# Optimization experiments

Measured on AMD Instinct MI355X. Metric: run time of the kernel, lower is better.

Reference implementation:

```python
import jax, jax.numpy as jnp
import numpy as np

# dims matching init_kwargs
B, N = 1, 2048
VOCAB, DIM, DEPTH = 32000, 1024, 4
HEADS, DIM_HEAD, WINDOW = 16, 64, 512
INNER = HEADS * DIM_HEAD          # 1024
FF_INNER = int(DIM * 4 * 2 / 3)   # 2730 (GEGLU inner)
DPB_DIM = DIM // 2
LN_EPS = 1e-5


def layernorm(x, g, b):
    m = jnp.mean(x, axis=-1, keepdims=True)
    v = jnp.mean(jnp.square(x - m), axis=-1, keepdims=True)
    return (x - m) * jax.lax.rsqrt(v + LN_EPS) * g + b


def look_around(x, backward=1, forward=0, pad_value=-1):
    # x: [b, nw, w, ...]; concat shifted windows along the window_size axis
    nw = x.shape[1]
    pads = [(0, 0), (backward, forward)] + [(0, 0)] * (x.ndim - 2)
    px = jnp.pad(x, pads, constant_values=pad_value)
    return jnp.concatenate([px[:, i:i + nw] for i in range(backward + forward + 1)], axis=2)


def dynamic_pos_bias(w1, b1, w2, b2, w3, b3, i, j):
    # MLP over scalar relative distances, then gather into [H, i, j]
    rel = jnp.arange(j, dtype=jnp.float32)[:, None]            # [j, 1]
    h = jax.nn.silu(rel @ w1 + b1)
    h = jax.nn.silu(h @ w2 + b2)
    bias = h @ w3 + b3                                          # [j, H]
    idx = jnp.abs(jnp.arange(j - i, j)[:, None] - jnp.arange(j)[None, :])  # [i, j]
    return jnp.transpose(bias[idx], (2, 0, 1))                  # [H, i, j]


def local_attention(q, k, v, attn_bias):
    # causal sliding-window attention, look_backward=1, look_forward=0, exact_windowsize=True
    # q,k,v: [B,H,N,dh]; N assumed multiple of WINDOW (autopad is a no-op then)
    b, h, n, d = q.shape
    w = WINDOW
    nw = n // w
    scale = d ** -0.5
    bq = q.reshape(b * h, nw, w, d) * scale
    bk = look_around(k.reshape(b * h, nw, w, d), pad_value=-1.0)   # [bh,nw,2w,d]
    bv = look_around(v.reshape(b * h, nw, w, d), pad_value=-1.0)
    t = jnp.arange(n).reshape(1, nw, w)
    bq_t = t[..., :, None]                                      # [1,nw,w,1]
    bq_k = look_around(t, pad_value=-1)[..., None, :]           # [1,nw,1,2w]
    # causal | exact-window | padding masks
    mask = (bq_t < bq_k) | (bq_t > bq_k + w) | (bq_k == -1)
    sim = jnp.einsum('bwid,bwjd->bwij', bq, bk)                 # [bh,nw,w,2w]
    sim = (sim.reshape(b, h, nw, w, 2 * w) + attn_bias[None, :, None]).reshape(b * h, nw, w, 2 * w)
    sim = jnp.where(mask, -jnp.finfo(sim.dtype).max, sim)
    attn = jax.nn.softmax(sim, axis=-1)
    out = jnp.einsum('bwij,bwjd->bwid', attn, bv)
    return out.reshape(b, h, n, d)


def forward(tokens, tok_emb, pos_emb, dpb_w1, dpb_b1, dpb_w2, dpb_b2, dpb_w3, dpb_b3,
            ln1_g, ln1_b, Wqkv, Wo, ln2_g, ln2_b, Wff1, Wff2, lnf_g, lnf_b, Wlogits):
    bsz, n = tokens.shape
    x = tok_emb[tokens] + pos_emb[:n]                           # [B,N,D]
    bias = dynamic_pos_bias(dpb_w1, dpb_b1, dpb_w2, dpb_b2, dpb_w3, dpb_b3, WINDOW, 2 * WINDOW)

    def split_heads(t):
        return t.reshape(bsz, n, HEADS, DIM_HEAD).transpose(0, 2, 1, 3)

    for l in range(DEPTH):
        # LocalMHA (prenorm) + residual
        h = layernorm(x, ln1_g[l], ln1_b[l])
        q, k, v = jnp.split(h @ Wqkv[l], 3, axis=-1)
        o = local_attention(split_heads(q), split_heads(k), split_heads(v), bias)
        o = o.transpose(0, 2, 1, 3).reshape(bsz, n, INNER)
        x = x + o @ Wo[l]
        # GEGLU FFN (prenorm inside FeedForward) + residual
        h = layernorm(x, ln2_g[l], ln2_b[l])
        a, gate = jnp.split(h @ Wff1[l], 2, axis=-1)
        x = x + (a * jax.nn.gelu(gate, approximate=False)) @ Wff2[l]

    return layernorm(x, lnf_g, lnf_b) @ Wlogits                 # [B,N,V]


def setup_inputs() -> dict:
    key = jax.random.key(0)
    ks = iter(jax.random.split(key, 16))
    s = 0.02
    rn = lambda *shape: jax.random.normal(next(ks), shape, dtype=jnp.float32) * s
    return {
        'tokens': jax.random.randint(next(ks), (B, N), 0, VOCAB, dtype=jnp.int32),
        'tok_emb': rn(VOCAB, DIM),
        'pos_emb': rn(N, DIM),
        'dpb_w1': rn(1, DPB_DIM), 'dpb_b1': jnp.zeros((DPB_DIM,), jnp.float32),
        'dpb_w2': rn(DPB_DIM, DPB_DIM), 'dpb_b2': jnp.zeros((DPB_DIM,), jnp.float32),
        'dpb_w3': rn(DPB_DIM, HEADS), 'dpb_b3': jnp.zeros((HEADS,), jnp.float32),
        'ln1_g': jnp.ones((DEPTH, DIM), jnp.float32), 'ln1_b': jnp.zeros((DEPTH, DIM), jnp.float32),
        'Wqkv': rn(DEPTH, DIM, 3 * INNER),
        'Wo': rn(DEPTH, INNER, DIM),
        'ln2_g': jnp.ones((DEPTH, DIM), jnp.float32), 'ln2_b': jnp.zeros((DEPTH, DIM), jnp.float32),
        'Wff1': rn(DEPTH, DIM, 2 * FF_INNER),
        'Wff2': rn(DEPTH, FF_INNER, DIM),
        'lnf_g': jnp.ones((DIM,), jnp.float32), 'lnf_b': jnp.zeros((DIM,), jnp.float32),
        'Wlogits': rn(DIM, VOCAB),
    }


def reference(tokens, tok_emb, pos_emb, dpb_w1, dpb_b1, dpb_w2, dpb_b2, dpb_w3, dpb_b3,
              ln1_g, ln1_b, Wqkv, Wo, ln2_g, ln2_b, Wff1, Wff2, lnf_g, lnf_b, Wlogits):
    return forward(tokens, tok_emb, pos_emb, dpb_w1, dpb_b1, dpb_w2, dpb_b2, dpb_w3, dpb_b3,
                   ln1_g, ln1_b, Wqkv, Wo, ln2_g, ln2_b, Wff1, Wff2, lnf_g, lnf_b, Wlogits)
```

## Files before the change

### kernel.cpp

```cpp
#include <hip/hip_runtime.h>
#include <cstdint>

#define DEV __device__ __forceinline__

typedef __attribute__((ext_vector_type(8))) short bf16x8;
typedef __attribute__((ext_vector_type(4))) short bf16x4;
typedef __attribute__((ext_vector_type(4))) float f32x4;
typedef __attribute__((ext_vector_type(8))) unsigned short u16x8;

DEV float bf2f(unsigned short u) { return __uint_as_float(((unsigned)u) << 16); }
DEV unsigned short f2bf(float f) {
  unsigned u = __float_as_uint(f);
  u += 0x7FFFu + ((u >> 16) & 1u);
  return (unsigned short)(u >> 16);
}

DEV void gload_lds16(const void* g, void* lds) {
  __builtin_amdgcn_global_load_lds(
      (const __attribute__((address_space(1))) unsigned int*)g,
      (__attribute__((address_space(3))) unsigned int*)lds, 16, 0, 0);
}

__global__ __launch_bounds__(256) void k_prep(
    const int* __restrict__ tokens, const float* __restrict__ tok_emb,
    const float* __restrict__ pos_emb, float* __restrict__ x,
    const float* __restrict__ w1, const float* __restrict__ b1,
    const float* __restrict__ w2, const float* __restrict__ b2,
    const float* __restrict__ w3, const float* __restrict__ b3,
    float* __restrict__ tableT,
    const float* __restrict__ Wqkv, unsigned short* __restrict__ WqkvT,
    const float* __restrict__ Wo, unsigned short* __restrict__ WoT,
    const float* __restrict__ Wff1, unsigned short* __restrict__ Wff1T,
    const float* __restrict__ Wff2, unsigned short* __restrict__ Wff2T,
    const float* __restrict__ Wlog, unsigned short* __restrict__ WlogT) {
  __shared__ unsigned short sm16[8192];
  int b = blockIdx.x, t = threadIdx.x;
  if (b < 2048) {
    int tok = tokens[b];
    int c = t * 4;
    float4 a = *(const float4*)(tok_emb + (long)tok * 1024 + c);
    float4 p = *(const float4*)(pos_emb + (long)b * 1024 + c);
    float4 r;
    r.x = a.x + p.x; r.y = a.y + p.y; r.z = a.z + p.z; r.w = a.w + p.w;
    *(float4*)(x + (long)b * 1024 + c) = r;
    return;
  }
  b -= 2048;
  if (b < 1024) {
    float* h1 = (float*)sm16;
    float* h2 = h1 + 512;
    float rf = (float)b;
    for (int c = t; c < 512; c += 256) {
      float v = rf * w1[c] + b1[c];
      h1[c] = v / (1.0f + __expf(-v));
    }
    __syncthreads();
    for (int c = t; c < 512; c += 256) {
      float acc = b2[c];
      for (int k2 = 0; k2 < 512; ++k2) acc = fmaf(h1[k2], w2[(long)k2 * 512 + c], acc);
      h2[c] = acc / (1.0f + __expf(-acc));
    }
    __syncthreads();
    if (t < 16) {
      float acc = b3[t];
      for (int k2 = 0; k2 < 512; ++k2) acc = fmaf(h2[k2], w3[k2 * 16 + t], acc);
      tableT[t * 1024 + b] = acc;
    }
    return;
  }
  b -= 1024;
  const float* src; unsigned short* dst;
  int N, Kreal, nt, kt, mode;
  if (b < 1536) {
    int z = b / 384, r = b % 384;
    nt = r / 16; kt = r % 16; mode = 0; N = 3072; Kreal = 1024;
    src = Wqkv + (long)z * 1024 * 3072;
    dst = WqkvT + ((long)z * 384 + r) * 8192;
  } else if ((b -= 1536) < 512) {
    int z = b / 128, r = b % 128;
    nt = r / 16; kt = r % 16; mode = 0; N = 1024; Kreal = 1024;
    src = Wo + (long)z * 1024 * 1024;
    dst = WoT + ((long)z * 128 + r) * 8192;
  } else if ((b -= 512) < 2752) {
    int z = b / 688, r = b % 688;
    nt = r / 16; kt = r % 16; mode = 1; N = 5460; Kreal = 1024;
    src = Wff1 + (long)z * 1024 * 5460;
    dst = Wff1T + ((long)z * 688 + r) * 8192;
  } else if ((b -= 2752) < 1376) {
    int z = b / 344, r = b % 344;
    nt = r / 43; kt = r % 43; mode = 0; N = 1024; Kreal = 2730;
    src = Wff2 + (long)z * 2730 * 1024;
    dst = Wff2T + ((long)z * 344 + r) * 8192;
  } else {
    b -= 1376;
    nt = b / 16; kt = b % 16; mode = 0; N = 32000; Kreal = 1024;
    src = Wlog;
    dst = WlogT + (long)b * 8192;
  }
  const int k0 = kt * 64;
  const int q = t & 31;
  const int kc = t >> 5;
  u16x8 pa, pb, pc, pd;
  if (mode == 0) {
    const int nb = nt * 128 + q * 4;
    float4 v[8];
#pragma unroll
    for (int e = 0; e < 8; ++e) {
      int k = k0 + kc * 8 + e;
      float4 tmp = {0.f, 0.f, 0.f, 0.f};
      if (k < Kreal) tmp = *(const float4*)(src + (long)k * N + nb);
      v[e] = tmp;
    }
    __builtin_amdgcn_sched_barrier(0);
#pragma unroll
    for (int e = 0; e < 8; ++e) {
      pa[e] = f2bf(v[e].x); pb[e] = f2bf(v[e].y);
      pc[e] = f2bf(v[e].z); pd[e] = f2bf(v[e].w);
    }
  } else {
    const int f0 = nt * 64 + q * 2;
    float2 av[8], gv[8];
#pragma unroll
    for (int e = 0; e < 8; ++e) {
      int k = k0 + kc * 8 + e;
      const float* sr = src + (long)k * 5460;
      float2 af = {0.f, 0.f}, gf = {0.f, 0.f};
      if (f0 + 1 < 2730) {
        af = *(const float2*)(sr + f0);
        gf = *(const float2*)(sr + 2730 + f0);
      } else if (f0 < 2730) {
        af.x = sr[f0];
        gf.x = sr[2730 + f0];
      }
      av[e] = af; gv[e] = gf;
    }
    __builtin_amdgcn_sched_barrier(0);
#pragma unroll
    for (int e = 0; e < 8; ++e) {
      pa[e] = f2bf(av[e].x); pb[e] = f2bf(gv[e].x);
      pc[e] = f2bf(av[e].y); pd[e] = f2bf(gv[e].y);
    }
  }
  {
    const int r0 = q * 4;
    *(u16x8*)&sm16[(r0 + 0) * 64 + ((kc ^ ((r0 + 0) & 7)) * 8)] = pa;
    *(u16x8*)&sm16[(r0 + 1) * 64 + ((kc ^ ((r0 + 1) & 7)) * 8)] = pb;
    *(u16x8*)&sm16[(r0 + 2) * 64 + ((kc ^ ((r0 + 2) & 7)) * 8)] = pc;
    *(u16x8*)&sm16[(r0 + 3) * 64 + ((kc ^ ((r0 + 3) & 7)) * 8)] = pd;
  }
  __syncthreads();
#pragma unroll
  for (int i2 = 0; i2 < 4; ++i2)
    *(u16x8*)(dst + i2 * 2048 + t * 8) = *(const u16x8*)&sm16[i2 * 2048 + t * 8];
}

__global__ __launch_bounds__(256) void k_ln4(const float* __restrict__ x,
    const float* __restrict__ g, const float* __restrict__ b,
    unsigned short* __restrict__ out) {
  const int row = blockIdx.x * 4 + (threadIdx.x >> 6);
  const int l = threadIdx.x & 63;
  const float* xr = x + (long)row * 1024 + l * 16;
  float4 v[4];
#pragma unroll
  for (int e = 0; e < 4; ++e) v[e] = ((const float4*)xr)[e];
  float s = 0.0f;
#pragma unroll
  for (int e = 0; e < 4; ++e) s += v[e].x + v[e].y + v[e].z + v[e].w;
#pragma unroll
  for (int off = 32; off; off >>= 1) s += __shfl_xor(s, off);
  float mean = s * (1.0f / 1024.0f);
  float sq = 0.0f;
#pragma unroll
  for (int e = 0; e < 4; ++e) {
    float a0 = v[e].x - mean, a1 = v[e].y - mean, a2 = v[e].z - mean, a3 = v[e].w - mean;
    sq += a0 * a0 + a1 * a1 + a2 * a2 + a3 * a3;
  }
#pragma unroll
  for (int off = 32; off; off >>= 1) sq += __shfl_xor(sq, off);
  float inv = rsqrtf(sq * (1.0f / 1024.0f) + 1e-5f);
  const float* gr = g + l * 16;
  const float* br = b + l * 16;
  unsigned short* orow = out + (long)row * 1024 + l * 16;
#pragma unroll
  for (int e = 0; e < 4; ++e) {
    float4 gv = ((const float4*)gr)[e];
    float4 bv = ((const float4*)br)[e];
    ushort4 o;
    o.x = f2bf((v[e].x - mean) * inv * gv.x + bv.x);
    o.y = f2bf((v[e].y - mean) * inv * gv.y + bv.y);
    o.z = f2bf((v[e].z - mean) * inv * gv.z + bv.z);
    o.w = f2bf((v[e].w - mean) * inv * gv.w + bv.w);
    ((ushort4*)orow)[e] = o;
  }
}

__global__ __launch_bounds__(256, 2) void k_attn_mfma(
    const unsigned short* __restrict__ qkv, const float* __restrict__ tableT,
    unsigned short* __restrict__ o) {
  __shared__ unsigned short Ks[64 * 64];
  __shared__ unsigned short Vt[64 * 72];
  __shared__ unsigned short Ps[4][16 * 72];
  __shared__ float biasl[1024];
  const int qt = blockIdx.x, h = blockIdx.y, wi = blockIdx.z;
  const int iw0 = qt * 64;
  const int t = threadIdx.x;
  const int w = t >> 6, l = t & 63;
  const int lq = l & 15, lk = l >> 4;

  *(float4*)&biasl[t * 4] = *(const float4*)(tableT + h * 1024 + t * 4);

  const unsigned short* qp = qkv + (long)(wi * 512 + iw0 + w * 16 + lq) * 3072 + h * 64;
  bf16x8 qf0 = *(const bf16x8*)(qp + lk * 8);
  bf16x8 qf1 = *(const bf16x8*)(qp + 32 + lk * 8);

  f32x4 oacc[4] = {};
  float mrun[4] = {-3.0e38f, -3.0e38f, -3.0e38f, -3.0e38f};
  float srun[4] = {};

  const int kt0 = (wi == 0) ? 8 : qt;
  const int kt1 = qt + 8;
  for (int kt = kt0; kt <= kt1; ++kt) {
    const int ktbase = kt * 64;
    const long kgbase = (long)((wi - 1) * 512 + ktbase);
    __syncthreads();
    {
      const unsigned short* Kg = qkv + kgbase * 3072 + 1024 + h * 64;
#pragma unroll
      for (int s2 = 0; s2 < 2; ++s2) {
        int g = s2 * 4 + w;
        int row = g * 8 + (l >> 3);
        int gch = (l & 7) ^ (row & 7);
        gload_lds16(Kg + (long)row * 3072 + gch * 8, &Ks[g * 512]);
      }
    }
    {
      int kp = t & 31, dg = t >> 5;
      const unsigned short* Vg =
          qkv + (kgbase + 2 * kp) * 3072 + 2048 + h * 64 + dg * 8;
      bf16x8 a0 = *(const bf16x8*)Vg;
      bf16x8 a1 = *(const bf16x8*)(Vg + 3072);
#pragma unroll
      for (int e = 0; e < 8; ++e) {
        unsigned pack = ((unsigned)(unsigned short)a0[e]) |
                        (((unsigned)(unsigned short)a1[e]) << 16);
        *(unsigned*)&Vt[(dg * 8 + e) * 72 + 2 * kp] = pack;
      }
    }
    asm volatile("s_waitcnt vmcnt(0)" ::: "memory");
    __syncthreads();

    f32x4 sacc[4] = {};
#pragma unroll
    for (int ct = 0; ct < 4; ++ct) {
      int krow = ct * 16 + lq;
      bf16x8 kf0 = *(const bf16x8*)&Ks[krow * 64 + (((0 + lk) ^ (krow & 7)) * 8)];
      bf16x8 kf1 = *(const bf16x8*)&Ks[krow * 64 + (((4 + lk) ^ (krow & 7)) * 8)];
      sacc[ct] = __builtin_amdgcn_mfma_f32_16x16x32_bf16(qf0, kf0, sacc[ct], 0, 0, 0);
      sacc[ct] = __builtin_amdgcn_mfma_f32_16x16x32_bf16(qf1, kf1, sacc[ct], 0, 0, 0);
    }

#pragma unroll
    for (int r = 0; r < 4; ++r) {
      const int iw = iw0 + w * 16 + lk * 4 + r;
      float sc[4];
#pragma unroll
      for (int ct = 0; ct < 4; ++ct) {
        int jj = ktbase + ct * 16 + lq;
        int di = 512 + iw - jj;
        int dic = min(max(di, 0), 1023);
        bool allowed = (jj >= iw) && (jj <= iw + 512);
        float v = sacc[ct][r] * 0.125f + biasl[dic];
        sc[ct] = allowed ? v : -3.0e38f;
      }
      float mx = fmaxf(fmaxf(sc[0], sc[1]), fmaxf(sc[2], sc[3]));
      mx = fmaxf(mx, __shfl_xor(mx, 1));
      mx = fmaxf(mx, __shfl_xor(mx, 2));
      mx = fmaxf(mx, __shfl_xor(mx, 4));
      mx = fmaxf(mx, __shfl_xor(mx, 8));
      float mnew = fmaxf(mrun[r], mx);
      float f = __expf(mrun[r] - mnew);
      mrun[r] = mnew;
      float rs = 0.0f;
#pragma unroll
      for (int ct = 0; ct < 4; ++ct) {
        float pv = __expf(sc[ct] - mnew);
        rs += pv;
        Ps[w][(lk * 4 + r) * 72 + ct * 16 + lq] = f2bf(pv);
      }
      rs += __shfl_xor(rs, 1);
      rs += __shfl_xor(rs, 2);
      rs += __shfl_xor(rs, 4);
      rs += __shfl_xor(rs, 8);
      srun[r] = srun[r] * f + rs;
#pragma unroll
      for (int dt = 0; dt < 4; ++dt) oacc[dt][r] *= f;
    }
    asm volatile("s_waitcnt lgkmcnt(0)" ::: "memory");

#pragma unroll
    for (int ks = 0; ks < 2; ++ks) {
      bf16x4 pa0 = *(const bf16x4*)&Ps[w][lq * 72 + ks * 32 + lk * 8];
      bf16x4 pa1 = *(const bf16x4*)&Ps[w][lq * 72 + ks * 32 + lk * 8 + 4];
      bf16x8 pa = __builtin_shufflevector(pa0, pa1, 0, 1, 2, 3, 4, 5, 6, 7);
#pragma unroll
      for (int dt = 0; dt < 4; ++dt) {
        int drow = dt * 16 + lq;
        bf16x4 vb0 = *(const bf16x4*)&Vt[drow * 72 + ks * 32 + lk * 8];
        bf16x4 vb1 = *(const bf16x4*)&Vt[drow * 72 + ks * 32 + lk * 8 + 4];
        bf16x8 vb = __builtin_shufflevector(vb0, vb1, 0, 1, 2, 3, 4, 5, 6, 7);
        oacc[dt] = __builtin_amdgcn_mfma_f32_16x16x32_bf16(pa, vb, oacc[dt], 0, 0, 0);
      }
    }
  }

  unsigned short* ob =
      o + (long)(wi * 512 + iw0 + w * 16 + lk * 4) * 1024 + h * 64 + lq;
#pragma unroll
  for (int r = 0; r < 4; ++r) {
    float inv = 1.0f / srun[r];
#pragma unroll
    for (int dt = 0; dt < 4; ++dt)
      ob[(long)r * 1024 + dt * 16] = f2bf(oacc[dt][r] * inv);
  }
}

template <int EPI, int BM>
__global__ __launch_bounds__(256, 2) void k_gemm(const unsigned short* __restrict__ A,
    const unsigned short* __restrict__ BTt, void* __restrict__ Cout,
    int N, int K, int nbm) {
  constexpr int MI = BM / 32;
  __shared__ unsigned short As[BM * 64];
  __shared__ unsigned short Bs[128 * 64];
  const int nwg = gridDim.x;
  const int orig = blockIdx.x;
  const int q8 = nwg >> 3, r8 = nwg & 7;
  const int xcd = orig & 7, i8 = orig >> 3;
  const int wgid = (xcd < r8 ? xcd * (q8 + 1) : r8 * (q8 + 1) + (xcd - r8) * q8) + i8;
  const int bm = wgid % nbm;
  const int bn = wgid / nbm;
  const int t = threadIdx.x;
  const int w = t >> 6, l = t & 63;
  const int wm = w >> 1, wn = w & 1;
  const int lrow = l >> 3, lch = l & 7;
  const int lq = l & 15, lk = l >> 4;
  f32x4 acc[MI][4] = {};
  const long arow0 = (long)bm * BM;
  const unsigned short* btile = BTt + (long)bn * (K >> 6) * 8192;
  for (int kt = 0; kt < K; kt += 64) {
    __syncthreads();
    const unsigned short* bsrc = btile + (long)(kt >> 6) * 8192 + l * 8;
#pragma unroll
    for (int s2 = 0; s2 < 4; ++s2) {
      int grp = s2 * 4 + w;
      gload_lds16(bsrc + grp * 512, &Bs[grp * 512]);
      if (s2 < MI) {
        int r = grp * 8 + lrow;
        int gch = lch ^ lrow;
        gload_lds16(A + (arow0 + r) * K + kt + gch * 8, &As[grp * 512]);
      }
    }
    asm volatile("s_waitcnt vmcnt(0)" ::: "memory");
    __syncthreads();
#pragma unroll
    for (int kk = 0; kk < 2; ++kk) {
      bf16x8 af[MI], bfr[4];
#pragma unroll
      for (int i = 0; i < MI; ++i) {
        int ra = wm * (BM / 2) + i * 16 + lq;
        af[i] = *(const bf16x8*)&As[ra * 64 + (((kk * 4 + lk) ^ (ra & 7)) * 8)];
      }
#pragma unroll
      for (int j = 0; j < 4; ++j) {
        int rb = wn * 64 + j * 16 + lq;
        bfr[j] = *(const bf16x8*)&Bs[rb * 64 + (((kk * 4 + lk) ^ (rb & 7)) * 8)];
      }
#pragma unroll
      for (int i = 0; i < MI; ++i)
#pragma unroll
        for (int j = 0; j < 4; ++j)
          acc[i][j] = __builtin_amdgcn_mfma_f32_16x16x32_bf16(af[i], bfr[j],
                                                              acc[i][j], 0, 0, 0);
    }
  }
  const int rbase = bm * BM + wm * (BM / 2) + lk * 4;
  const int cbase = bn * 128 + wn * 64 + lq;
#pragma unroll
  for (int i = 0; i < MI; ++i) {
#pragma unroll
    for (int j = 0; j < 4; ++j) {
#pragma unroll
      for (int r2 = 0; r2 < 4; ++r2) {
        long row = rbase + i * 16 + r2;
        long col = cbase + j * 16;
        float v = acc[i][j][r2];
        if (EPI == 0) {
          ((unsigned short*)Cout)[row * N + col] = f2bf(v);
        } else if (EPI == 1) {
          ((float*)Cout)[row * N + col] += v;
        } else if (EPI == 2) {
          ((float*)Cout)[row * N + col] = v;
        } else {
          float gpart = __shfl_xor(v, 1);
          if ((lq & 1) == 0) {
            float uval =
                v * (0.5f * gpart * (1.0f + erff(gpart * 0.70710678118654752f)));
            ((unsigned short*)Cout)[row * (N >> 1) + (col >> 1)] = f2bf(uval);
          }
        }
      }
    }
  }
}

extern "C" void kernel_launch(void* const* d_in, const int* in_sizes, int n_in,
                              void* d_out, int out_size, void* d_ws, size_t ws_size,
                              hipStream_t stream) {
  (void)in_sizes; (void)n_in; (void)out_size; (void)ws_size;
  const int* tokens   = (const int*)d_in[0];
  const float* tok_emb = (const float*)d_in[1];
  const float* pos_emb = (const float*)d_in[2];
  const float* dpb_w1 = (const float*)d_in[3];
  const float* dpb_b1 = (const float*)d_in[4];
  const float* dpb_w2 = (const float*)d_in[5];
  const float* dpb_b2 = (const float*)d_in[6];
  const float* dpb_w3 = (const float*)d_in[7];
  const float* dpb_b3 = (const float*)d_in[8];
  const float* ln1_g  = (const float*)d_in[9];
  const float* ln1_b  = (const float*)d_in[10];
  const float* Wqkv   = (const float*)d_in[11];
  const float* Wo     = (const float*)d_in[12];
  const float* ln2_g  = (const float*)d_in[13];
  const float* ln2_b  = (const float*)d_in[14];
  const float* Wff1   = (const float*)d_in[15];
  const float* Wff2   = (const float*)d_in[16];
  const float* lnf_g  = (const float*)d_in[17];
  const float* lnf_b  = (const float*)d_in[18];
  const float* Wlog   = (const float*)d_in[19];
  float* out = (float*)d_out;

  char* p = (char*)d_ws;
  auto carve = [&](size_t bytes) {
    char* q = p;
    p += (bytes + 255) & ~(size_t)255;
    return (void*)q;
  };
  unsigned short* WqkvT = (unsigned short*)carve((size_t)4 * 3072 * 1024 * 2);
  unsigned short* WoT   = (unsigned short*)carve((size_t)4 * 1024 * 1024 * 2);
  unsigned short* Wff1T = (unsigned short*)carve((size_t)4 * 5504 * 1024 * 2);
  unsigned short* Wff2T = (unsigned short*)carve((size_t)4 * 1024 * 2752 * 2);
  unsigned short* WlogT = (unsigned short*)carve((size_t)32000 * 1024 * 2);
  float*          x     = (float*)carve((size_t)2048 * 1024 * 4);
  unsigned short* hbuf  = (unsigned short*)carve((size_t)2048 * 1024 * 2);
  unsigned short* qkv   = (unsigned short*)carve((size_t)2048 * 3072 * 2);
  unsigned short* ao    = (unsigned short*)carve((size_t)2048 * 1024 * 2);
  unsigned short* ubuf  = (unsigned short*)carve((size_t)2048 * 2752 * 2);
  float*          tableT = (float*)carve((size_t)16 * 1024 * 4);

  k_prep<<<13248, 256, 0, stream>>>(
      tokens, tok_emb, pos_emb, x, dpb_w1, dpb_b1, dpb_w2, dpb_b2, dpb_w3,
      dpb_b3, tableT, Wqkv, WqkvT, Wo, WoT, Wff1, Wff1T, Wff2, Wff2T, Wlog, WlogT);

  for (int l = 0; l < 4; ++l) {
    k_ln4<<<512, 256, 0, stream>>>(x, ln1_g + l * 1024, ln1_b + l * 1024, hbuf);
    k_gemm<0, 64><<<dim3(32 * (3072 / 128)), 256, 0, stream>>>(
        hbuf, WqkvT + (long)l * 3072 * 1024, qkv, 3072, 1024, 32);
    k_attn_mfma<<<dim3(8, 16, 4), 256, 0, stream>>>(qkv, tableT, ao);
    k_gemm<1, 64><<<dim3(32 * (1024 / 128)), 256, 0, stream>>>(
        ao, WoT + (long)l * 1024 * 1024, x, 1024, 1024, 32);
    k_ln4<<<512, 256, 0, stream>>>(x, ln2_g + l * 1024, ln2_b + l * 1024, hbuf);
    k_gemm<3, 128><<<dim3(16 * (5504 / 128)), 256, 0, stream>>>(
        hbuf, Wff1T + (long)l * 5504 * 1024, ubuf, 5504, 1024, 16);
    k_gemm<1, 64><<<dim3(32 * (1024 / 128)), 256, 0, stream>>>(
        ubuf, Wff2T + (long)l * 1024 * 2752, x, 1024, 2752, 32);
  }
  k_ln4<<<512, 256, 0, stream>>>(x, lnf_g, lnf_b, hbuf);
  k_gemm<2, 128><<<dim3(16 * (32000 / 128)), 256, 0, stream>>>(
      hbuf, WlogT, out, 32000, 1024, 16);
}
```

Baseline: 1.027 ms.

## Add 256x128 tile, 8-wave triple-buffered GEMM for the logits projection

Adds a new GEMM kernel with 512 threads, a 256x128 output tile, triple-buffered LDS staging through direct global-to-LDS loads, and XCD-aware workgroup remapping. It is used only for the final 2048x32000 logits projection in place of the 128-row tile kernel. The larger M tile halves how often each weight tile is re-read and gives more MFMA work per barrier. In exchange the kernel uses about 144KB of LDS, which caps occupancy at one block per CU.

```diff
diff --git a/kernel.cpp b/kernel.cpp
--- a/kernel.cpp
+++ b/kernel.cpp
@@ -412,6 +412,95 @@
   }
 }
 
+__global__ __launch_bounds__(512) void k_gemm8(
+    const unsigned short* __restrict__ A, const unsigned short* __restrict__ BTt,
+    float* __restrict__ Cout, int N, int K, int nbm) {
+  __shared__ unsigned short As[3][256 * 64];
+  __shared__ unsigned short Bs[3][128 * 64];
+  const int nwg = gridDim.x;
+  const int orig = blockIdx.x;
+  const int q8 = nwg >> 3, r8 = nwg & 7;
+  const int xcd = orig & 7, i8 = orig >> 3;
+  const int wgid = (xcd < r8 ? xcd * (q8 + 1) : r8 * (q8 + 1) + (xcd - r8) * q8) + i8;
+  const int bm = wgid % nbm;
+  const int bn = wgid / nbm;
+  const int t = threadIdx.x;
+  const int w8 = t >> 6, l = t & 63;
+  const int wm = w8 >> 1, wn = w8 & 1;
+  const int lrow = l >> 3, lch = l & 7;
+  const int lq = l & 15, lk = l >> 4;
+  f32x4 acc[4][4] = {};
+  const long arow0 = (long)bm * 256;
+  const int NT = K >> 6;
+  const unsigned short* btile = BTt + (long)bn * NT * 8192;
+  const int gch = lch ^ lrow;
+
+  auto STAGE = [&](int buf, int kt) {
+    const unsigned short* bsrc = btile + (long)kt * 8192 + l * 8;
+#pragma unroll
+    for (int s = 0; s < 2; ++s) {
+      int grp = s * 8 + w8;
+      gload_lds16(bsrc + grp * 512, &Bs[buf][grp * 512]);
+    }
+#pragma unroll
+    for (int s = 0; s < 4; ++s) {
+      int grp = s * 8 + w8;
+      int row = grp * 8 + lrow;
+      gload_lds16(A + (arow0 + row) * K + kt * 64 + gch * 8, &As[buf][grp * 512]);
+    }
+  };
+
+  STAGE(0, 0);
+  if (NT > 1) STAGE(1, 1);
+  asm volatile("s_waitcnt vmcnt(6)" ::: "memory");
+  __builtin_amdgcn_s_barrier();
+  for (int kt = 0; kt < NT; ++kt) {
+    const int buf = kt % 3;
+    if (kt + 2 < NT) STAGE((kt + 2) % 3, kt + 2);
+#pragma unroll
+    for (int kk = 0; kk < 2; ++kk) {
+      bf16x8 af[4], bfr[4];
+#pragma unroll
+      for (int i = 0; i < 4; ++i) {
+        int ra = wm * 64 + i * 16 + lq;
+        af[i] = *(const bf16x8*)&As[buf][ra * 64 + (((kk * 4 + lk) ^ (ra & 7)) * 8)];
+      }
+#pragma unroll
+      for (int j = 0; j < 4; ++j) {
+        int rb = wn * 64 + j * 16 + lq;
+        bfr[j] = *(const bf16x8*)&Bs[buf][rb * 64 + (((kk * 4 + lk) ^ (rb & 7)) * 8)];
+      }
+#pragma unroll
+      for (int i = 0; i < 4; ++i)
+#pragma unroll
+        for (int j = 0; j < 4; ++j)
+          acc[i][j] = __builtin_amdgcn_mfma_f32_16x16x32_bf16(af[i], bfr[j],
+                                                              acc[i][j], 0, 0, 0);
+    }
+    if (kt + 1 < NT) {
+      if (kt + 2 < NT)
+        asm volatile("s_waitcnt vmcnt(6)" ::: "memory");
+      else
+        asm volatile("s_waitcnt vmcnt(0)" ::: "memory");
+      __builtin_amdgcn_s_barrier();
+    }
+  }
+  const int rbase = bm * 256 + wm * 64 + lk * 4;
+  const int cbase = bn * 128 + wn * 64 + lq;
+#pragma unroll
+  for (int i = 0; i < 4; ++i) {
+#pragma unroll
+    for (int j = 0; j < 4; ++j) {
+#pragma unroll
+      for (int r2 = 0; r2 < 4; ++r2) {
+        long row = rbase + i * 16 + r2;
+        long col = cbase + j * 16;
+        Cout[row * N + col] = acc[i][j][r2];
+      }
+    }
+  }
+}
+
 extern "C" void kernel_launch(void* const* d_in, const int* in_sizes, int n_in,
                               void* d_out, int out_size, void* d_ws, size_t ws_size,
                               hipStream_t stream) {
@@ -474,6 +563,5 @@
         ubuf, Wff2T + (long)l * 1024 * 2752, x, 1024, 2752, 32);
   }
   k_ln4<<<512, 256, 0, stream>>>(x, lnf_g, lnf_b, hbuf);
-  k_gemm<2, 128><<<dim3(16 * (32000 / 128)), 256, 0, stream>>>(
-      hbuf, WlogT, out, 32000, 1024, 16);
-}
+  k_gemm8<<<2000, 512, 0, stream>>>(hbuf, WlogT, out, 32000, 1024, 8);
+}
```

Result: slower. 1.103 ms (+7.3%).
